# Kernel optimization log

Hardware: AMD Instinct MI355X
Metric: run time of the kernel (lower is better)

## Reference

```python
import jax, jax.numpy as jnp
import numpy as np

B, L, E, H = 4, 2048, 1024, 16
HD = E // H  # 64
ROPE_BASE = 10000.0


def setup_inputs() -> dict:
    key = jax.random.key(0)
    ks = jax.random.split(key, 4)
    x = jax.random.normal(ks[0], (B, L, E), dtype=jnp.float32)
    Wqkv = jax.random.normal(ks[1], (3 * E, E), dtype=jnp.float32) * (E ** -0.5)
    bqkv = jnp.zeros((3 * E,), dtype=jnp.float32)
    Wout = jax.random.normal(ks[2], (E, E), dtype=jnp.float32) * (E ** -0.5)
    bout = jnp.zeros((E,), dtype=jnp.float32)
    # RoPE tables: (1, 1, L, HD/2)
    half = HD // 2
    inv_freq = 1.0 / (ROPE_BASE ** (jnp.arange(half, dtype=jnp.float32) / half))
    t = jnp.arange(L, dtype=jnp.float32)
    freqs = t[:, None] * inv_freq[None, :]  # (L, half)
    cos = jnp.cos(freqs)[None, None]
    sin = jnp.sin(freqs)[None, None]
    return {"x": x, "cos": cos, "sin": sin, "Wqkv": Wqkv, "bqkv": bqkv,
            "Wout": Wout, "bout": bout}


def _apply_rope(q, k, cos, sin):
    half = q.shape[-1] // 2
    q1, q2 = q[..., :half], q[..., half:]
    k1, k2 = k[..., :half], k[..., half:]
    q_rot = jnp.concatenate([q1 * cos - q2 * sin, q1 * sin + q2 * cos], axis=-1)
    k_rot = jnp.concatenate([k1 * cos - k2 * sin, k1 * sin + k2 * cos], axis=-1)
    return q_rot, k_rot


def reference(x, cos, sin, Wqkv, bqkv, Wout, bout):
    b, l, e = x.shape
    qkv = x @ Wqkv.T + bqkv  # (B, L, 3E)
    q, k, v = jnp.split(qkv, 3, axis=-1)
    # (B, H, L, HD)
    q = q.reshape(b, l, H, HD).transpose(0, 2, 1, 3)
    k = k.reshape(b, l, H, HD).transpose(0, 2, 1, 3)
    v = v.reshape(b, l, H, HD).transpose(0, 2, 1, 3)
    q, k = _apply_rope(q, k, cos, sin)
    scale = 1.0 / jnp.sqrt(jnp.asarray(HD, dtype=x.dtype))
    scores = jnp.einsum('bhqd,bhkd->bhqk', q, k) * scale
    attn = jax.nn.softmax(scores, axis=-1)
    out = jnp.einsum('bhqk,bhkd->bhqd', attn, v)  # (B, H, L, HD)
    out = out.transpose(0, 2, 1, 3).reshape(b, l, e)
    out = out @ Wout.T + bout
    return out
```

## Files before the change

### kernel.cpp

```cpp
#include <hip/hip_runtime.h>
#include <math.h>

#define B 4
#define L 2048
#define E 1024
#define H 16
#define HD 64
#define MROWS (B*L)
#define E3 (3*E)

using bf16x8   = __attribute__((ext_vector_type(8))) short;
using f16x8    = __attribute__((ext_vector_type(8))) _Float16;
using floatx4  = __attribute__((ext_vector_type(4))) float;
using floatx16 = __attribute__((ext_vector_type(16))) float;

__device__ inline ushort f2bf(float x) {
    uint u = __float_as_uint(x);
    u += 0x7FFF + ((u >> 16) & 1);
    return (ushort)(u >> 16);
}
__device__ inline float bf2f(ushort h) { return __uint_as_float(((uint)h) << 16); }
__device__ inline ushort f2h(float x) { _Float16 h = (_Float16)x; return *(ushort*)&h; }

#if __has_builtin(__builtin_amdgcn_exp2f)
#define EXP2F(x) __builtin_amdgcn_exp2f(x)
#else
#define EXP2F(x) exp2f(x)
#endif

__device__ inline void async16(const void* g, void* l) {
    __builtin_amdgcn_global_load_lds(
        (const __attribute__((address_space(1))) uint*)g,
        (__attribute__((address_space(3))) uint*)l, 16, 0, 0);
}

__device__ inline uint pack_rtz(float odd, float even) {
    return __builtin_amdgcn_perm(__float_as_uint(odd), __float_as_uint(even), 0x07060302u);
}

#define VMW(n) asm volatile("s_waitcnt vmcnt(" #n ")" ::: "memory")
#define SBAR() asm volatile("s_barrier" ::: "memory")

#define N1Q ((size_t)MROWS * E / 4)
#define N2Q ((size_t)E3 * E / 4)
#define N3Q ((size_t)E * E / 4)
__global__ __launch_bounds__(256) void cvt_all(
        const float* __restrict__ x, const float* __restrict__ wq,
        const float* __restrict__ wo, ushort* __restrict__ x16,
        ushort* __restrict__ wq16, ushort* __restrict__ wo16)
{
    size_t i = (size_t)blockIdx.x * 256 + threadIdx.x;
    const float* src; ushort* dst; size_t j;
    if (i < N1Q)                  { src = x;  dst = x16;  j = i; }
    else if (i < N1Q + N2Q)       { src = wq; dst = wq16; j = i - N1Q; }
    else                          { src = wo; dst = wo16; j = i - N1Q - N2Q; }
    float4 v = ((const float4*)src)[j];
    ushort4 o;
    o.x = f2h(v.x); o.y = f2h(v.y); o.z = f2h(v.z); o.w = f2h(v.w);
    ((ushort4*)dst)[j] = o;
}

template<int MODE, int MF>
__global__ __launch_bounds__(512, 2) void gemm256(
        const ushort* __restrict__ A16, const ushort* __restrict__ B16,
        const float* __restrict__ bias, float* __restrict__ Cf,
        ushort* __restrict__ qh, ushort* __restrict__ kh, ushort* __restrict__ vT,
        const float* __restrict__ cosT, const float* __restrict__ sinT,
        int Ndim, int Kdim)
{
    constexpr int BM    = MF * 32;
    constexpr int ACOLS = MF * 1024;
    constexpr int SLOT  = ACOLS + 8192;
    constexpr int AP    = MF / 4;
    __shared__ ushort lds[4][SLOT];

    const int tid  = threadIdx.x;
    const int w    = tid >> 6, lane = tid & 63;
    const int g    = lane >> 4, c = lane & 15;
    const int wm   = w >> 2,  wn = w & 3;

    const int gx  = gridDim.x;
    const int nwg = gx * gridDim.y;
    int bid = blockIdx.y * gx + blockIdx.x;
    bid = (bid & 7) * (nwg >> 3) + (bid >> 3);
    const int m0 = (bid / gx) * BM;
    const int n0 = (bid % gx) * 256;

    const int rl = lane >> 2, q = lane & 3;
    const ushort* srcA[AP]; int dstA[AP];
#pragma unroll
    for (int p = 0; p < AP; ++p) {
        const int row = (w * AP + p) * 16 + rl;
        const int kg  = q ^ ((row >> 1) & 3);
        srcA[p] = A16 + (size_t)(m0 + row) * Kdim + kg * 8;
        dstA[p] = (w * AP + p) * 512;
    }
    const ushort* srcB[2]; int dstB[2];
#pragma unroll
    for (int p = 0; p < 2; ++p) {
        const int n  = (w * 2 + p) * 16 + rl;
        const int kg = q ^ ((n >> 1) & 3);
        srcB[p] = B16 + (size_t)(n0 + n) * Kdim + kg * 8;
        dstB[p] = ACOLS + (w * 2 + p) * 512;
    }

    int scount = 0;
    auto stage = [&]() {
        ushort* base = &lds[scount & 3][0];
#pragma unroll
        for (int p = 0; p < AP; ++p) { async16(srcA[p], base + dstA[p]); srcA[p] += 32; }
#pragma unroll
        for (int p = 0; p < 2; ++p) { async16(srcB[p], base + dstB[p]); srcB[p] += 32; }
        ++scount;
    };

    floatx4 acc[MF][4];
#pragma unroll
    for (int m = 0; m < MF; ++m)
#pragma unroll
        for (int n = 0; n < 4; ++n) acc[m][n] = (floatx4){0.f, 0.f, 0.f, 0.f};

    const int swz   = (g ^ ((c >> 1) & 3)) << 3;
    const int baseA = (wm * (MF * 16) + c) * 32 + swz;
    const int baseB = ACOLS + (wn * 64 + c) * 32 + swz;

    auto compute = [&](int sl) {
        const ushort* cur = &lds[sl][0];
        f16x8 af[MF], bf[4];
#pragma unroll
        for (int m = 0; m < MF; ++m) af[m] = *(const f16x8*)&cur[baseA + m * 512];
#pragma unroll
        for (int n = 0; n < 4; ++n)  bf[n] = *(const f16x8*)&cur[baseB + n * 512];
        __builtin_amdgcn_s_setprio(1);
#pragma unroll
        for (int m = 0; m < MF; ++m)
#pragma unroll
            for (int n = 0; n < 4; ++n)
                acc[m][n] = __builtin_amdgcn_mfma_f32_16x16x32_f16(af[m], bf[n], acc[m][n], 0, 0, 0);
        __builtin_amdgcn_s_setprio(0);
    };

    const int NKH = Kdim >> 5;

    stage();
    stage();

    for (int h = 0; h < NKH - 2; ++h) {
        stage();
        if constexpr (MF == 8) VMW(8); else VMW(6);
        SBAR();
        compute(h & 3);
    }
    if constexpr (MF == 8) VMW(4); else VMW(3);
    SBAR();
    compute((NKH - 2) & 3);
    VMW(0);
    SBAR();
    compute((NKH - 1) & 3);

    const int colbase = n0 + wn * 64;
#pragma unroll
    for (int fm = 0; fm < MF; ++fm) {
        const int rowb = m0 + wm * (MF * 16) + fm * 16 + g * 4;
        if constexpr (MODE == 2) {
#pragma unroll
            for (int i = 0; i < 4; ++i) {
                const int row = rowb + i;
#pragma unroll
                for (int nt = 0; nt < 4; ++nt) {
                    const int col = colbase + nt * 16 + c;
                    Cf[(size_t)row * Ndim + col] = acc[fm][nt][i] + bias[col];
                }
            }
        } else {
            const int sec = colbase >> 10;
            const int hg  = (colbase & 1023) >> 6;
#pragma unroll
            for (int i = 0; i < 4; ++i) {
                const int row = rowb + i;
                const int bb = row >> 11;
                const int l  = row & (L - 1);
                if (sec < 2) {
                    ushort* dst = (sec == 0 ? qh : kh) + ((size_t)(bb * H + hg) * L + l) * HD;
                    const int sw = l & 7;
                    const float qs = (sec == 0) ? 0.18033688f : 1.0f;
#pragma unroll
                    for (int nt = 0; nt < 2; ++nt) {
                        const int d  = nt * 16 + c;
                        const int d2 = d + 32;
                        float v1 = acc[fm][nt][i]     + bias[colbase + d];
                        float v2 = acc[fm][nt + 2][i] + bias[colbase + d2];
                        float cs = cosT[l * 32 + d], sn = sinT[l * 32 + d];
                        dst[(((d  >> 3) ^ sw) << 3) | (d  & 7)] = f2bf((v1 * cs - v2 * sn) * qs);
                        dst[(((d2 >> 3) ^ sw) << 3) | (d2 & 7)] = f2bf((v1 * sn + v2 * cs) * qs);
                    }
                } else {
                    const int lp = (l & ~12) | ((l & 4) << 1) | ((l & 8) >> 1);
                    const int intile = ((((lp >> 3) & 7)) << 3);
#pragma unroll
                    for (int nt = 0; nt < 4; ++nt) {
                        const int d = nt * 16 + c;
                        float v = acc[fm][nt][i] + bias[colbase + d];
                        size_t idx = ((size_t)(bb * H + hg) * HD + d) * L
                                   + (l & ~63) + (intile ^ ((d & 7) << 3)) + (lp & 7);
                        vT[idx] = f2bf(v);
                    }
                }
            }
        }
    }
}

__global__ __launch_bounds__(256, 4) void flash_mfma4(
        const ushort* __restrict__ qh, const ushort* __restrict__ kh,
        const ushort* __restrict__ vT, ushort* __restrict__ attn16)
{
    __shared__ ushort Ks[2][4096];
    __shared__ ushort Vt[2][4096];

    const int tid  = threadIdx.x;
    const int w    = tid >> 6;
    const int lane = tid & 63;
    const int h    = lane >> 5;
    const int n    = lane & 31;
    const int b    = blockIdx.x >> 4;
    const int hd   = blockIdx.x & 15;
    const int q0   = blockIdx.y * 128;

    const ushort* khead = kh + (size_t)(b * H + hd) * L * HD;
    const ushort* vhead = vT + (size_t)(b * H + hd) * HD * L;

    const int q = q0 + 32 * w + n;
    const ushort* qrow = qh + ((size_t)(b * H + hd) * L + q) * HD;
    bf16x8 aq[4];
#pragma unroll
    for (int kd = 0; kd < 4; ++kd)
        aq[kd] = *(const bf16x8*)&qrow[((2 * kd + h) ^ (q & 7)) << 3];

    const int wk = w & 1;
    const ushort* ksrc = khead + (size_t)(32 * wk) * 64 + lane * 8;
    const ushort* vsrc = vhead + (size_t)(32 * wk + (lane >> 3)) * L + (lane & 7) * 8;

    const int NIT = L / 64;
    if (w < 2) {
#pragma unroll
        for (int p = 0; p < 4; ++p)
            async16(ksrc + p * 512, &Ks[0][32 * wk * 64 + p * 512]);
    } else {
#pragma unroll
        for (int p = 0; p < 4; ++p)
            async16(vsrc + (size_t)p * 8 * L, &Vt[0][32 * wk * 64 + p * 512]);
    }

    float l_i = 0.f;
    floatx16 o[2];
    o[0] = (floatx16)(0.f);
    o[1] = (floatx16)(0.f);

    for (int it = 0; it < NIT; ++it) {
        const int p = it & 1;
        __syncthreads();

        if (it + 1 < NIT) {
            if (w < 2) {
                const ushort* s = ksrc + (size_t)(it + 1) * 4096;
#pragma unroll
                for (int pp = 0; pp < 4; ++pp)
                    async16(s + pp * 512, &Ks[p ^ 1][32 * wk * 64 + pp * 512]);
            } else {
                const ushort* s = vsrc + (size_t)(it + 1) * 64;
#pragma unroll
                for (int pp = 0; pp < 4; ++pp)
                    async16(s + (size_t)pp * 8 * L, &Vt[p ^ 1][32 * wk * 64 + pp * 512]);
            }
        }

        const ushort* KsC = Ks[p];
        const ushort* VtC = Vt[p];

#pragma unroll
        for (int js = 0; js < 2; ++js) {
            floatx16 s = (floatx16)(-16.0f);
#pragma unroll
            for (int kd = 0; kd < 4; ++kd) {
                bf16x8 kf = *(const bf16x8*)&KsC[(32 * js + n) * 64 + (((2 * kd + h) ^ (n & 7)) << 3)];
                s = __builtin_amdgcn_mfma_f32_32x32x16_bf16(kf, aq[kd], s, 0, 0, 0);
            }

            float pv[16];
            float rs = 0.f;
#pragma unroll
            for (int rr = 0; rr < 4; ++rr) {
                float p0 = EXP2F(s[4 * rr + 0]);
                float p1 = EXP2F(s[4 * rr + 1]);
                float p2 = EXP2F(s[4 * rr + 2]);
                float p3 = EXP2F(s[4 * rr + 3]);
                pv[4 * rr + 0] = p0; pv[4 * rr + 1] = p1;
                pv[4 * rr + 2] = p2; pv[4 * rr + 3] = p3;
                rs += (p0 + p1) + (p2 + p3);
            }
            l_i += rs;

#pragma unroll
            for (int f = 0; f < 2; ++f) {
                uint bu[4];
                bu[0] = pack_rtz(pv[8 * f + 1], pv[8 * f + 0]);
                bu[1] = pack_rtz(pv[8 * f + 3], pv[8 * f + 2]);
                bu[2] = pack_rtz(pv[8 * f + 5], pv[8 * f + 4]);
                bu[3] = pack_rtz(pv[8 * f + 7], pv[8 * f + 6]);
                bf16x8 bp = *(const bf16x8*)&bu[0];
#pragma unroll
                for (int nt = 0; nt < 2; ++nt) {
                    bf16x8 vf = *(const bf16x8*)&VtC[(32 * nt + n) * 64 + (((4 * js + 2 * f + h) ^ (n & 7)) << 3)];
                    o[nt] = __builtin_amdgcn_mfma_f32_32x32x16_bf16(vf, bp, o[nt], 0, 0, 0);
                }
            }
        }
    }

    const float l_tot = l_i + __shfl_xor(l_i, 32, 64);
    const float inv = 1.f / l_tot;
    const size_t rowbase = ((size_t)(b * L + q)) * E + hd * HD;
#pragma unroll
    for (int nt = 0; nt < 2; ++nt)
#pragma unroll
        for (int rr = 0; rr < 4; ++rr) {
            const int d0 = 32 * nt + 8 * rr + 4 * h;
            ushort h0 = f2h(o[nt][4 * rr + 0] * inv);
            ushort h1 = f2h(o[nt][4 * rr + 1] * inv);
            ushort h2 = f2h(o[nt][4 * rr + 2] * inv);
            ushort h3 = f2h(o[nt][4 * rr + 3] * inv);
            uint2 hw;
            hw.x = (uint)h0 | ((uint)h1 << 16);
            hw.y = (uint)h2 | ((uint)h3 << 16);
            *(uint2*)&attn16[rowbase + d0] = hw;
        }
}

extern "C" void kernel_launch(void* const* d_in, const int* in_sizes, int n_in,
                              void* d_out, int out_size, void* d_ws, size_t ws_size,
                              hipStream_t stream) {
    const float* x    = (const float*)d_in[0];
    const float* cosT = (const float*)d_in[1];
    const float* sinT = (const float*)d_in[2];
    const float* Wqkv = (const float*)d_in[3];
    const float* bqkv = (const float*)d_in[4];
    const float* Wout = (const float*)d_in[5];
    const float* bout = (const float*)d_in[6];
    float* out = (float*)d_out;

    const size_t NX = (size_t)MROWS * E;
    ushort* us   = (ushort*)d_ws;
    ushort* qh   = us;
    ushort* kh   = us + NX;
    ushort* vTp  = us + 2 * NX;
    ushort* x16  = us + 3 * NX;
    ushort* at16 = us + 4 * NX;
    ushort* wq16 = us + 5 * NX;
    ushort* wo16 = wq16 + (size_t)E3 * E;

    const int cvt_blocks = (int)((N1Q + N2Q + N3Q + 255) / 256);
    cvt_all<<<cvt_blocks, 256, 0, stream>>>(x, Wqkv, Wout, x16, wq16, wo16);

    gemm256<1, 8><<<dim3(E3 / 256, MROWS / 256), 512, 0, stream>>>(
        x16, wq16, bqkv, nullptr, qh, kh, vTp, cosT, sinT, E3, E);

    flash_mfma4<<<dim3(B * H, L / 128), 256, 0, stream>>>(qh, kh, vTp, at16);

    gemm256<2, 4><<<dim3(E / 256, MROWS / 128), 512, 0, stream>>>(
        at16, wo16, bout, out, nullptr, nullptr, nullptr, nullptr, nullptr, E, E);
}
```

Baseline: 290.1 us.

## Rework GEMMs into 4-wave 256x128 tiles with split-phase prefetch pipeline

Replaces the 8-wave 256x256 (and 128x256) GEMM kernels with a single 4-wave kernel computing 256x128 tiles, each wave owning a 128x64 sub-tile. The K loop now uses a 3-slot LDS ring and splits each step into two halves. In each half, LDS fragment reads and the A or B prefetch are interleaved with MFMA groups, separated by barriers and sched_barrier. The intent is better overlap of global loads, LDS reads and MFMA work, plus more work per wave. The cost is more barriers per step and a different grid shape and occupancy for both projections.

```diff
diff --git a/kernel.cpp b/kernel.cpp
--- a/kernel.cpp
+++ b/kernel.cpp
@@ -38,8 +38,10 @@
     return __builtin_amdgcn_perm(__float_as_uint(odd), __float_as_uint(even), 0x07060302u);
 }
 
-#define VMW(n) asm volatile("s_waitcnt vmcnt(" #n ")" ::: "memory")
-#define SBAR() asm volatile("s_barrier" ::: "memory")
+#define VMW(n)  asm volatile("s_waitcnt vmcnt(" #n ")" ::: "memory")
+#define LGKM0() asm volatile("s_waitcnt lgkmcnt(0)" ::: "memory")
+#define SBAR()  __builtin_amdgcn_s_barrier()
+#define SCHED0() __builtin_amdgcn_sched_barrier(0)
 
 #define N1Q ((size_t)MROWS * E / 4)
 #define N2Q ((size_t)E3 * E / 4)
@@ -60,40 +62,39 @@
     ((ushort4*)dst)[j] = o;
 }
 
-template<int MODE, int MF>
-__global__ __launch_bounds__(512, 2) void gemm256(
+template<int MODE>
+__global__ __launch_bounds__(256, 2) void gemm4w(
         const ushort* __restrict__ A16, const ushort* __restrict__ B16,
         const float* __restrict__ bias, float* __restrict__ Cf,
         ushort* __restrict__ qh, ushort* __restrict__ kh, ushort* __restrict__ vT,
         const float* __restrict__ cosT, const float* __restrict__ sinT,
         int Ndim, int Kdim)
 {
-    constexpr int BM    = MF * 32;
-    constexpr int ACOLS = MF * 1024;
-    constexpr int SLOT  = ACOLS + 8192;
-    constexpr int AP    = MF / 4;
-    __shared__ ushort lds[4][SLOT];
+    constexpr int BM    = 256;
+    constexpr int ACOLS = BM * 32;
+    constexpr int SLOT  = ACOLS + 4096;
+    __shared__ ushort lds[3][SLOT];
 
     const int tid  = threadIdx.x;
     const int w    = tid >> 6, lane = tid & 63;
     const int g    = lane >> 4, c = lane & 15;
-    const int wm   = w >> 2,  wn = w & 3;
+    const int wm   = w >> 1,  wn = w & 1;
 
     const int gx  = gridDim.x;
     const int nwg = gx * gridDim.y;
     int bid = blockIdx.y * gx + blockIdx.x;
     bid = (bid & 7) * (nwg >> 3) + (bid >> 3);
     const int m0 = (bid / gx) * BM;
-    const int n0 = (bid % gx) * 256;
+    const int n0 = (bid % gx) * 128;
 
     const int rl = lane >> 2, q = lane & 3;
-    const ushort* srcA[AP]; int dstA[AP];
-#pragma unroll
-    for (int p = 0; p < AP; ++p) {
-        const int row = (w * AP + p) * 16 + rl;
+    const ushort* srcA[4]; int dstA[4];
+#pragma unroll
+    for (int p = 0; p < 4; ++p) {
+        const int row = (w * 4 + p) * 16 + rl;
         const int kg  = q ^ ((row >> 1) & 3);
         srcA[p] = A16 + (size_t)(m0 + row) * Kdim + kg * 8;
-        dstA[p] = (w * AP + p) * 512;
+        dstA[p] = (w * 4 + p) * 512;
     }
     const ushort* srcB[2]; int dstB[2];
 #pragma unroll
@@ -104,64 +105,79 @@
         dstB[p] = ACOLS + (w * 2 + p) * 512;
     }
 
-    int scount = 0;
-    auto stage = [&]() {
-        ushort* base = &lds[scount & 3][0];
-#pragma unroll
-        for (int p = 0; p < AP; ++p) { async16(srcA[p], base + dstA[p]); srcA[p] += 32; }
+    auto stageA = [&](ushort* base) {
+#pragma unroll
+        for (int p = 0; p < 4; ++p) { async16(srcA[p], base + dstA[p]); srcA[p] += 32; }
+    };
+    auto stageB = [&](ushort* base) {
 #pragma unroll
         for (int p = 0; p < 2; ++p) { async16(srcB[p], base + dstB[p]); srcB[p] += 32; }
-        ++scount;
     };
 
-    floatx4 acc[MF][4];
-#pragma unroll
-    for (int m = 0; m < MF; ++m)
+    floatx4 acc[8][4];
+#pragma unroll
+    for (int m = 0; m < 8; ++m)
 #pragma unroll
         for (int n = 0; n < 4; ++n) acc[m][n] = (floatx4){0.f, 0.f, 0.f, 0.f};
 
     const int swz   = (g ^ ((c >> 1) & 3)) << 3;
-    const int baseA = (wm * (MF * 16) + c) * 32 + swz;
+    const int baseA = (wm * 128 + c) * 32 + swz;
     const int baseB = ACOLS + (wn * 64 + c) * 32 + swz;
 
-    auto compute = [&](int sl) {
-        const ushort* cur = &lds[sl][0];
-        f16x8 af[MF], bf[4];
-#pragma unroll
-        for (int m = 0; m < MF; ++m) af[m] = *(const f16x8*)&cur[baseA + m * 512];
-#pragma unroll
-        for (int n = 0; n < 4; ++n)  bf[n] = *(const f16x8*)&cur[baseB + n * 512];
+    const int NKH = Kdim >> 5;
+
+    stageA(&lds[0][0]); stageB(&lds[0][0]);
+    stageA(&lds[1][0]); stageB(&lds[1][0]);
+    VMW(6);
+    SBAR();
+
+    int cs = 0, ts = 2;
+    for (int h = 0; h < NKH; ++h) {
+        const ushort* cur = &lds[cs][0];
+        const bool pre = (h + 2 < NKH);
+        f16x8 af[8], bf[4];
+
+#pragma unroll
+        for (int m = 0; m < 4; ++m) af[m] = *(const f16x8*)&cur[baseA + m * 512];
+#pragma unroll
+        for (int n = 0; n < 4; ++n) bf[n] = *(const f16x8*)&cur[baseB + n * 512];
+        if (pre) stageA(&lds[ts][0]);
+        SBAR();
+        LGKM0();
+        SCHED0();
         __builtin_amdgcn_s_setprio(1);
 #pragma unroll
-        for (int m = 0; m < MF; ++m)
+        for (int m = 0; m < 4; ++m)
 #pragma unroll
             for (int n = 0; n < 4; ++n)
                 acc[m][n] = __builtin_amdgcn_mfma_f32_16x16x32_f16(af[m], bf[n], acc[m][n], 0, 0, 0);
         __builtin_amdgcn_s_setprio(0);
-    };
-
-    const int NKH = Kdim >> 5;
-
-    stage();
-    stage();
-
-    for (int h = 0; h < NKH - 2; ++h) {
-        stage();
-        if constexpr (MF == 8) VMW(8); else VMW(6);
         SBAR();
-        compute(h & 3);
-    }
-    if constexpr (MF == 8) VMW(4); else VMW(3);
-    SBAR();
-    compute((NKH - 2) & 3);
-    VMW(0);
-    SBAR();
-    compute((NKH - 1) & 3);
+
+#pragma unroll
+        for (int m = 4; m < 8; ++m) af[m] = *(const f16x8*)&cur[baseA + m * 512];
+        if (pre) { stageB(&lds[ts][0]); VMW(6); }
+        else if (h == NKH - 2) { VMW(0); }
+        SBAR();
+        LGKM0();
+        SCHED0();
+        __builtin_amdgcn_s_setprio(1);
+#pragma unroll
+        for (int m = 4; m < 8; ++m)
+#pragma unroll
+            for (int n = 0; n < 4; ++n)
+                acc[m][n] = __builtin_amdgcn_mfma_f32_16x16x32_f16(af[m], bf[n], acc[m][n], 0, 0, 0);
+        __builtin_amdgcn_s_setprio(0);
+        SBAR();
+
+        cs = (cs == 2) ? 0 : cs + 1;
+        ts = (ts == 2) ? 0 : ts + 1;
+    }
 
     const int colbase = n0 + wn * 64;
 #pragma unroll
-    for (int fm = 0; fm < MF; ++fm) {
-        const int rowb = m0 + wm * (MF * 16) + fm * 16 + g * 4;
+    for (int fm = 0; fm < 8; ++fm) {
+        const int rowb = m0 + wm * 128 + fm * 16 + g * 4;
         if constexpr (MODE == 2) {
 #pragma unroll
             for (int i = 0; i < 4; ++i) {
@@ -190,9 +206,9 @@
                         const int d2 = d + 32;
                         float v1 = acc[fm][nt][i]     + bias[colbase + d];
                         float v2 = acc[fm][nt + 2][i] + bias[colbase + d2];
-                        float cs = cosT[l * 32 + d], sn = sinT[l * 32 + d];
-                        dst[(((d  >> 3) ^ sw) << 3) | (d  & 7)] = f2bf((v1 * cs - v2 * sn) * qs);
-                        dst[(((d2 >> 3) ^ sw) << 3) | (d2 & 7)] = f2bf((v1 * sn + v2 * cs) * qs);
+                        float cs2 = cosT[l * 32 + d], sn = sinT[l * 32 + d];
+                        dst[(((d  >> 3) ^ sw) << 3) | (d  & 7)] = f2bf((v1 * cs2 - v2 * sn) * qs);
+                        dst[(((d2 >> 3) ^ sw) << 3) | (d2 & 7)] = f2bf((v1 * sn + v2 * cs2) * qs);
                     }
                 } else {
                     const int lp = (l & ~12) | ((l & 4) << 1) | ((l & 8) >> 1);
@@ -362,11 +378,11 @@
     const int cvt_blocks = (int)((N1Q + N2Q + N3Q + 255) / 256);
     cvt_all<<<cvt_blocks, 256, 0, stream>>>(x, Wqkv, Wout, x16, wq16, wo16);
 
-    gemm256<1, 8><<<dim3(E3 / 256, MROWS / 256), 512, 0, stream>>>(
+    gemm4w<1><<<dim3(E3 / 128, MROWS / 256), 256, 0, stream>>>(
         x16, wq16, bqkv, nullptr, qh, kh, vTp, cosT, sinT, E3, E);
 
     flash_mfma4<<<dim3(B * H, L / 128), 256, 0, stream>>>(qh, kh, vTp, at16);
 
-    gemm256<2, 4><<<dim3(E / 256, MROWS / 128), 512, 0, stream>>>(
+    gemm4w<2><<<dim3(E / 128, MROWS / 256), 256, 0, stream>>>(
         at16, wo16, bout, out, nullptr, nullptr, nullptr, nullptr, nullptr, E, E);
 }
```

Measured after the change: 293.1 us. About the same (+1.0%).
